# Kernel optimization log

Measured on AMD Instinct MI355X. Metric: run time of the kernel, lower is better.

The kernel has to match this reference:

```python
import jax, jax.numpy as jnp
import numpy as np

B, T, C, H = 8, 2048, 384, 64

def setup_inputs() -> dict:
    key = jax.random.key(0)
    k1, k2, k3, k4 = jax.random.split(key, 4)
    x = jax.random.normal(k1, (B, T, C), dtype=jnp.float32)
    Wq = jax.random.normal(k2, (C, H), dtype=jnp.float32) * (C ** -0.5)
    Wk = jax.random.normal(k3, (C, H), dtype=jnp.float32) * (C ** -0.5)
    Wv = jax.random.normal(k4, (C, H), dtype=jnp.float32) * (C ** -0.5)
    return {"x": x, "Wq": Wq, "Wk": Wk, "Wv": Wv}

def reference(x, Wq, Wk, Wv):
    # x: (B, T, C); projections: (B, T, H)
    Bn, Tn, Cn = x.shape
    q = jnp.einsum('btc,ch->bth', x, Wq)
    k = jnp.einsum('btc,ch->bth', x, Wk)
    v = jnp.einsum('btc,ch->bth', x, Wv)
    # NOTE: source scales by C**-0.5 (embedding dim), not head_size**-0.5
    weights = jnp.einsum('bth,bsh->bts', q, k) * (Cn ** -0.5)  # (B, T, T)
    causal = jnp.tril(jnp.ones((Tn, Tn), dtype=bool))
    weights = jnp.where(causal, weights, -jnp.inf)
    # NOTE: source applies softmax over dim=1 (query/row axis), reproduced faithfully
    weights = jax.nn.softmax(weights, axis=1)
    # dropout omitted (eval-mode reference)
    return jnp.einsum('bts,bsh->bth', weights, v)
```

## Files before the change

kernel.cpp:

```cpp
#include <hip/hip_runtime.h>
#include <hip/hip_bf16.h>
#include <math.h>

#define Bn 8
#define Tn 2048
#define Cn 384
#define Hn 64
#define SCALE2 0.07362241f

using bf16x8 = __attribute__((ext_vector_type(8))) short;
using f32x4  = __attribute__((ext_vector_type(4))) float;
using u32x4  = __attribute__((ext_vector_type(4))) unsigned;

#define MFMA(a, b, c) __builtin_amdgcn_mfma_f32_16x16x32_bf16((a), (b), (c), 0, 0, 0)

static __device__ __forceinline__ short f2bf(float f) {
  unsigned u = __float_as_uint(f);
  u += 0x7fffu + ((u >> 16) & 1u);
  return (short)(u >> 16);
}
static __device__ __forceinline__ float bf2f(short s) {
  return __uint_as_float(((unsigned)(unsigned short)s) << 16);
}
static __device__ __forceinline__ float fexp2(float x) {
#if __has_builtin(__builtin_amdgcn_exp2f)
  return __builtin_amdgcn_exp2f(x);
#else
  return exp2f(x);
#endif
}
static __device__ __forceinline__ float frcp(float x) {
#if __has_builtin(__builtin_amdgcn_rcpf)
  return __builtin_amdgcn_rcpf(x);
#else
  return 1.0f / x;
#endif
}
static __device__ __forceinline__ unsigned pack2(float lo, float hi) {
  return (unsigned)(unsigned short)f2bf(lo) | ((unsigned)(unsigned short)f2bf(hi) << 16);
}
static __device__ __forceinline__ bf16x8 ldp(const unsigned* p) {
  u32x4 t; t[0] = p[0]; t[1] = p[1]; t[2] = p[2]; t[3] = p[3];
  return __builtin_bit_cast(bf16x8, t);
}

__global__ __launch_bounds__(256) void wconv_kernel(
    const float* __restrict__ Wq, const float* __restrict__ Wk,
    const float* __restrict__ Wv, short* __restrict__ WbT,
    float* __restrict__ Lsum) {
  int idx = blockIdx.x * 256 + threadIdx.x;
  if (idx < Bn * Tn) Lsum[idx] = 0.f;
  int n = idx / 384, k = idx - n * 384;
  const float* W = (n < 64) ? Wq : (n < 128) ? Wk : Wv;
  WbT[idx] = f2bf(W[k * 64 + (n & 63)]);
}

__global__ __launch_bounds__(256) void proj_kernel(
    const float* __restrict__ x, const short* __restrict__ WbT,
    short* __restrict__ qb, short* __restrict__ kb, short* __restrict__ vT) {
  __shared__ short xs[16][392];
  __shared__ short vtile[64][20];
  const int tid = threadIdx.x;
  const int t0 = blockIdx.x * 16;
  const float* xb = x + (size_t)t0 * Cn;
  #pragma unroll
  for (int i = 0; i < 6; ++i) {
    int j = tid + i * 256;
    int row = j / 96, colv = (j - row * 96) * 4;
    float4 v = *(const float4*)(xb + row * Cn + colv);
    short4 s4; s4.x = f2bf(v.x); s4.y = f2bf(v.y); s4.z = f2bf(v.z); s4.w = f2bf(v.w);
    *(short4*)(&xs[row][colv]) = s4;
  }
  __syncthreads();
  const int w = tid >> 6, l15 = tid & 15, quad = (tid & 63) >> 4;
  f32x4 acc[3] = {};
  for (int ks = 0; ks < 12; ++ks) {
    bf16x8 a = *(const bf16x8*)(&xs[l15][ks * 32 + quad * 8]);
    #pragma unroll
    for (int cf = 0; cf < 3; ++cf) {
      bf16x8 bfr = *(const bf16x8*)(WbT + (size_t)(48 * w + 16 * cf + l15) * Cn + ks * 32 + quad * 8);
      acc[cf] = MFMA(a, bfr, acc[cf]);
    }
  }
  #pragma unroll
  for (int cf = 0; cf < 3; ++cf) {
    int cbase = 48 * w + 16 * cf, c = cbase + l15;
    #pragma unroll
    for (int r = 0; r < 4; ++r) {
      int row = t0 + quad * 4 + r;
      short val = f2bf(acc[cf][r]);
      if (cbase < 64)       qb[(size_t)row * Hn + c] = val;
      else if (cbase < 128) kb[(size_t)row * Hn + (c - 64)] = val;
      else                  vtile[c - 128][quad * 4 + r] = val;
    }
  }
  __syncthreads();
  const int b = t0 >> 11, t0l = t0 & 2047;
  int h = tid >> 2, tseg = (tid & 3) * 4;
  *(short4*)(vT + ((size_t)(b * Hn + h)) * Tn + t0l + tseg) =
      *(const short4*)(&vtile[h][tseg]);
}

__global__ __launch_bounds__(256) void colstats_kernel(
    const short* __restrict__ qb, const short* __restrict__ kb,
    float* __restrict__ Lsum) {
  const int unit = ((blockIdx.x & 7) << 7) | (blockIdx.x >> 3);
  const int b = unit >> 7, rem = unit & 127;
  const int j = rem >> 3, u = rem & 7;
  const int lo = (u * 33) >> 3, hi = ((u + 1) * 33) >> 3;
  const int big = 32 - j;
  const int tid = threadIdx.x, w = tid >> 6, l15 = tid & 15, quad = (tid & 63) >> 4;
  __shared__ float redl[64][17];

  auto run = [&](const int i, const int k0, const int k1) {
    const int s0 = i << 6;
    float l[4] = {0.f, 0.f, 0.f, 0.f};
    const int n = k1 - k0;
    if (n > 0) {
      bf16x8 bk[8];
      #pragma unroll
      for (int nf = 0; nf < 4; ++nf) {
        const size_t krow = (size_t)(b * Tn + s0 + 16 * nf + l15) * Hn;
        bk[2 * nf]     = *(const bf16x8*)(kb + krow + quad * 8);
        bk[2 * nf + 1] = *(const bf16x8*)(kb + krow + 32 + quad * 8);
      }
      auto cload = [&](bf16x8& A0, bf16x8& A1, int k) {
        size_t ar = (size_t)(b * Tn + ((i + k) << 6) + 16 * w + l15) * Hn;
        A0 = *(const bf16x8*)(qb + ar + quad * 8);
        A1 = *(const bf16x8*)(qb + ar + 32 + quad * 8);
      };
      auto ccomp = [&](bf16x8 A0, bf16x8 A1, int k) {
        f32x4 sc[4] = {};
        #pragma unroll
        for (int nf = 0; nf < 4; ++nf) {
          sc[nf] = MFMA(A0, bk[2 * nf], sc[nf]);
          sc[nf] = MFMA(A1, bk[2 * nf + 1], sc[nf]);
        }
        const bool diag = (k == 0);
        const int tb = ((i + k) << 6) + 16 * w + quad * 4;
        #pragma unroll
        for (int nf = 0; nf < 4; ++nf) {
          int s = s0 + 16 * nf + l15;
          #pragma unroll
          for (int r = 0; r < 4; ++r) {
            float v = sc[nf][r] * SCALE2;
            if (diag && (tb + r) < s) v = -INFINITY;
            l[nf] += fexp2(v);
          }
        }
      };
      bf16x8 a0A, a1A, a0B, a1B, a0C, a1C;
      cload(a0A, a1A, k0);
      if (n > 1) cload(a0B, a1B, k0 + 1);
      if (n > 2) cload(a0C, a1C, k0 + 2);
      int k = k0;
      while (k + 3 < k1) {
        ccomp(a0A, a1A, k);     cload(a0A, a1A, k + 3);
        ccomp(a0B, a1B, k + 1); if (k + 4 < k1) cload(a0B, a1B, k + 4);
        ccomp(a0C, a1C, k + 2); if (k + 5 < k1) cload(a0C, a1C, k + 5);
        k += 3;
      }
      const int rem2 = k1 - k;
      if (rem2 > 0) ccomp(a0A, a1A, k);
      if (rem2 > 1) ccomp(a0B, a1B, k + 1);
      if (rem2 > 2) ccomp(a0C, a1C, k + 2);
    }
    __syncthreads();
    #pragma unroll
    for (int nf = 0; nf < 4; ++nf) redl[16 * nf + l15][w * 4 + quad] = l[nf];
    __syncthreads();
    if (tid < 64) {
      float ls = 0.f;
      #pragma unroll
      for (int q2 = 0; q2 < 16; ++q2) ls += redl[tid][q2];
      atomicAdd(&Lsum[b * Tn + s0 + tid], ls);
    }
  };
  run(j, lo, min(hi, big));
  run(31 - j, max(lo, big) - big, hi - big);
}

__global__ __launch_bounds__(256, 2) void outg_kernel(
    const short* __restrict__ qb, const short* __restrict__ kb,
    const short* __restrict__ vT, const float* __restrict__ Lsum,
    float* __restrict__ out) {
  const int bid = blockIdx.x;
  const int b = bid & 7;
  const int rest = bid >> 3;
  const int tile = 31 - (rest >> 1);
  const int half = rest & 1;
  const int nch = tile + 1;
  const int tid = threadIdx.x, w = tid >> 6, l15 = tid & 15, quad = (tid & 63) >> 4;
  __shared__ unsigned plds[4][512];
  __shared__ float red[4][32][64];
  __shared__ float rcpl[2048];

  const int smax = nch << 6;
  for (int s = tid; s < smax; s += 256)
    rcpl[s] = frcp(Lsum[b * Tn + s]);
  __syncthreads();

  const int swz = (l15 & 7) << 4;
  int wroff[8];
  #pragma unroll
  for (int nf = 0; nf < 4; ++nf)
    #pragma unroll
    for (int p = 0; p < 2; ++p)
      wroff[2 * nf + p] = (l15 * 128 + ((nf * 32 + quad * 8 + p * 4) ^ swz)) >> 2;
  const int rd0 = (l15 * 128 + ((quad * 16) ^ swz)) >> 2;
  const int rd1 = (l15 * 128 + ((64 + quad * 16) ^ swz)) >> 2;
  const size_t QKbase = (size_t)b * Tn * Hn;
  const size_t Vbase  = (size_t)b * Hn * Tn;
  const int tbase = (tile << 6) + (half << 5);
  const int tg0 = tbase + l15;
  const int tg1 = tbase + 16 + l15;

  const size_t qrow0 = QKbase + (size_t)(tbase + l15) * Hn;
  const size_t qrow1 = qrow0 + 16 * Hn;
  const bf16x8 qf00 = *(const bf16x8*)(qb + qrow0 + quad * 8);
  const bf16x8 qf01 = *(const bf16x8*)(qb + qrow0 + 32 + quad * 8);
  const bf16x8 qf10 = *(const bf16x8*)(qb + qrow1 + quad * 8);
  const bf16x8 qf11 = *(const bf16x8*)(qb + qrow1 + 32 + quad * 8);

  f32x4 acc0[4] = {}, acc1[4] = {};
  bf16x8 kfA[8], kfB[8], vf[8];
  auto loadK = [&](bf16x8 (&kf)[8], int ch) {
    const int s0 = ch << 6;
    #pragma unroll
    for (int nf = 0; nf < 4; ++nf) {
      const size_t kr = QKbase + (size_t)(s0 + 16 * nf + l15) * Hn;
      kf[2 * nf]     = *(const bf16x8*)(kb + kr + quad * 8);
      kf[2 * nf + 1] = *(const bf16x8*)(kb + kr + 32 + quad * 8);
    }
  };
  auto loadV = [&](int ch) {
    const int s0 = ch << 6;
    #pragma unroll
    for (int nf = 0; nf < 4; ++nf) {
      const size_t vr = Vbase + (size_t)(16 * nf + l15) * Tn + s0;
      vf[2 * nf]     = *(const bf16x8*)(vT + vr + quad * 8);
      vf[2 * nf + 1] = *(const bf16x8*)(vT + vr + 32 + quad * 8);
    }
  };
  auto strip = [&](const f32x4 (&sc)[4], const float (&rl)[16], int s0,
                   bool diag, int tg, f32x4 (&acc)[4]) {
    #pragma unroll
    for (int nf = 0; nf < 4; ++nf) {
      float ev[4];
      #pragma unroll
      for (int r = 0; r < 4; ++r) {
        float v = sc[nf][r] * SCALE2;
        const int s = s0 + 16 * nf + quad * 4 + r;
        if (diag && tg < s) v = -INFINITY;
        ev[r] = fexp2(v) * rl[nf * 4 + r];
      }
      plds[w][wroff[2 * nf]]     = pack2(ev[0], ev[1]);
      plds[w][wroff[2 * nf + 1]] = pack2(ev[2], ev[3]);
    }
    const bf16x8 a0 = ldp(&plds[w][rd0]);
    const bf16x8 a1 = ldp(&plds[w][rd1]);
    __builtin_amdgcn_s_setprio(1);
    #pragma unroll
    for (int nf = 0; nf < 4; ++nf) {
      acc[nf] = MFMA(a0, vf[2 * nf], acc[nf]);
      acc[nf] = MFMA(a1, vf[2 * nf + 1], acc[nf]);
    }
    __builtin_amdgcn_s_setprio(0);
  };
  auto body = [&](int ch, const bf16x8 (&CUR)[8], bf16x8 (&NXT)[8]) {
    const int s0 = ch << 6;
    const int nx = ch + 4;
    f32x4 sc0[4] = {}, sc1[4] = {};
    __builtin_amdgcn_s_setprio(1);
    #pragma unroll
    for (int nf = 0; nf < 4; ++nf) {
      sc0[nf] = MFMA(CUR[2 * nf], qf00, sc0[nf]);
      sc0[nf] = MFMA(CUR[2 * nf + 1], qf01, sc0[nf]);
    }
    #pragma unroll
    for (int nf = 0; nf < 4; ++nf) {
      sc1[nf] = MFMA(CUR[2 * nf], qf10, sc1[nf]);
      sc1[nf] = MFMA(CUR[2 * nf + 1], qf11, sc1[nf]);
    }
    __builtin_amdgcn_s_setprio(0);
    if (nx < nch) loadK(NXT, nx);
    float rl[16];
    #pragma unroll
    for (int nf = 0; nf < 4; ++nf)
      #pragma unroll
      for (int r = 0; r < 4; ++r)
        rl[nf * 4 + r] = rcpl[s0 + 16 * nf + quad * 4 + r];
    const bool diag = (ch == tile);
    strip(sc0, rl, s0, diag, tg0, acc0);
    strip(sc1, rl, s0, diag, tg1, acc1);
    if (nx < nch) loadV(nx);
  };

  if (w < nch) { loadK(kfA, w); loadV(w); }
  for (int ch = w; ch < nch; ch += 8) {
    body(ch, kfA, kfB);
    if (ch + 4 < nch) body(ch + 4, kfB, kfA);
  }

  #pragma unroll
  for (int nf = 0; nf < 4; ++nf)
    #pragma unroll
    for (int r = 0; r < 4; ++r) {
      red[w][quad * 4 + r][16 * nf + l15]      = acc0[nf][r];
      red[w][16 + quad * 4 + r][16 * nf + l15] = acc1[nf][r];
    }
  __syncthreads();
  {
    const int row = tid >> 3, c8 = (tid & 7) * 8;
    float4 t0 = {0.f, 0.f, 0.f, 0.f}, t1 = {0.f, 0.f, 0.f, 0.f};
    #pragma unroll
    for (int ww = 0; ww < 4; ++ww) {
      float4 s0 = *(const float4*)(&red[ww][row][c8]);
      float4 s1 = *(const float4*)(&red[ww][row][c8 + 4]);
      t0.x += s0.x; t0.y += s0.y; t0.z += s0.z; t0.w += s0.w;
      t1.x += s1.x; t1.y += s1.y; t1.z += s1.z; t1.w += s1.w;
    }
    float* o = &out[QKbase + (size_t)(tbase + row) * Hn + c8];
    *(float4*)(o) = t0;
    *(float4*)(o + 4) = t1;
  }
}

extern "C" void kernel_launch(void* const* d_in, const int* in_sizes, int n_in,
                              void* d_out, int out_size, void* d_ws, size_t ws_size,
                              hipStream_t stream) {
  const float* x  = (const float*)d_in[0];
  const float* Wq = (const float*)d_in[1];
  const float* Wk = (const float*)d_in[2];
  const float* Wv = (const float*)d_in[3];
  char* ws = (char*)d_ws;
  short* qb   = (short*)(ws);
  short* kb   = (short*)(ws + 2097152);
  short* vT   = (short*)(ws + 4194304);
  short* WbT  = (short*)(ws + 6291456);
  float* Lsum = (float*)(ws + 6438912);
  float* outp = (float*)d_out;

  hipLaunchKernelGGL(wconv_kernel, dim3(288), dim3(256), 0, stream, Wq, Wk, Wv, WbT, Lsum);
  hipLaunchKernelGGL(proj_kernel, dim3(Bn * Tn / 16), dim3(256), 0, stream, x, WbT, qb, kb, vT);
  hipLaunchKernelGGL(colstats_kernel, dim3(1024), dim3(256), 0, stream, qb, kb, Lsum);
  hipLaunchKernelGGL(outg_kernel, dim3(512), dim3(256), 0, stream, qb, kb, vT, Lsum, outp);
}
```

Measured before the change: 132.0 us.

## Fold softmax scale into Wq, split colstats finer, shorten prefetch ring

Multiplies Wq by the scale (including log2e) during weight conversion, so the per-score multiply is dropped in both the column-stats and output kernels. The column-stats kernel gets a 2048-block grid with 16 chunks per row-tile, a launch bound of two blocks per unit, a two-deep instead of three-deep q prefetch ring, and raised priority around its MFMA block. It also adds LDS alignment and removes an unused helper. Rounding q to bf16 after scaling slightly changes numerics, and the finer split adds more atomics and duplicate K-fragment loads.

```diff
diff --git a/kernel.cpp b/kernel.cpp
--- a/kernel.cpp
+++ b/kernel.cpp
@@ -18,9 +18,6 @@
   unsigned u = __float_as_uint(f);
   u += 0x7fffu + ((u >> 16) & 1u);
   return (short)(u >> 16);
-}
-static __device__ __forceinline__ float bf2f(short s) {
-  return __uint_as_float(((unsigned)(unsigned short)s) << 16);
 }
 static __device__ __forceinline__ float fexp2(float x) {
 #if __has_builtin(__builtin_amdgcn_exp2f)
@@ -52,7 +49,9 @@
   if (idx < Bn * Tn) Lsum[idx] = 0.f;
   int n = idx / 384, k = idx - n * 384;
   const float* W = (n < 64) ? Wq : (n < 128) ? Wk : Wv;
-  WbT[idx] = f2bf(W[k * 64 + (n & 63)]);
+  float wv = W[k * 64 + (n & 63)];
+  if (n < 64) wv *= SCALE2;
+  WbT[idx] = f2bf(wv);
 }
 
 __global__ __launch_bounds__(256) void proj_kernel(
@@ -101,13 +100,14 @@
       *(const short4*)(&vtile[h][tseg]);
 }
 
-__global__ __launch_bounds__(256) void colstats_kernel(
+__global__ __launch_bounds__(256, 2) void colstats_kernel(
     const short* __restrict__ qb, const short* __restrict__ kb,
     float* __restrict__ Lsum) {
-  const int unit = ((blockIdx.x & 7) << 7) | (blockIdx.x >> 3);
-  const int b = unit >> 7, rem = unit & 127;
-  const int j = rem >> 3, u = rem & 7;
-  const int lo = (u * 33) >> 3, hi = ((u + 1) * 33) >> 3;
+  const int bid = blockIdx.x;
+  const int b = bid & 7;
+  const int rem = bid >> 3;
+  const int j = rem >> 4, u = rem & 15;
+  const int lo = (u * 33) >> 4, hi = ((u + 1) * 33) >> 4;
   const int big = 32 - j;
   const int tid = threadIdx.x, w = tid >> 6, l15 = tid & 15, quad = (tid & 63) >> 4;
   __shared__ float redl[64][17];
@@ -131,11 +131,13 @@
       };
       auto ccomp = [&](bf16x8 A0, bf16x8 A1, int k) {
         f32x4 sc[4] = {};
+        __builtin_amdgcn_s_setprio(1);
         #pragma unroll
         for (int nf = 0; nf < 4; ++nf) {
           sc[nf] = MFMA(A0, bk[2 * nf], sc[nf]);
           sc[nf] = MFMA(A1, bk[2 * nf + 1], sc[nf]);
         }
+        __builtin_amdgcn_s_setprio(0);
         const bool diag = (k == 0);
         const int tb = ((i + k) << 6) + 16 * w + quad * 4;
         #pragma unroll
@@ -143,27 +145,23 @@
           int s = s0 + 16 * nf + l15;
           #pragma unroll
           for (int r = 0; r < 4; ++r) {
-            float v = sc[nf][r] * SCALE2;
+            float v = sc[nf][r];
             if (diag && (tb + r) < s) v = -INFINITY;
             l[nf] += fexp2(v);
           }
         }
       };
-      bf16x8 a0A, a1A, a0B, a1B, a0C, a1C;
+      bf16x8 a0A, a1A, a0B, a1B;
       cload(a0A, a1A, k0);
       if (n > 1) cload(a0B, a1B, k0 + 1);
-      if (n > 2) cload(a0C, a1C, k0 + 2);
       int k = k0;
-      while (k + 3 < k1) {
-        ccomp(a0A, a1A, k);     cload(a0A, a1A, k + 3);
-        ccomp(a0B, a1B, k + 1); if (k + 4 < k1) cload(a0B, a1B, k + 4);
-        ccomp(a0C, a1C, k + 2); if (k + 5 < k1) cload(a0C, a1C, k + 5);
-        k += 3;
+      while (k + 2 < k1) {
+        ccomp(a0A, a1A, k);     cload(a0A, a1A, k + 2);
+        ccomp(a0B, a1B, k + 1); if (k + 3 < k1) cload(a0B, a1B, k + 3);
+        k += 2;
       }
-      const int rem2 = k1 - k;
-      if (rem2 > 0) ccomp(a0A, a1A, k);
-      if (rem2 > 1) ccomp(a0B, a1B, k + 1);
-      if (rem2 > 2) ccomp(a0C, a1C, k + 2);
+      if (k < k1)     ccomp(a0A, a1A, k);
+      if (k + 1 < k1) ccomp(a0B, a1B, k + 1);
     }
     __syncthreads();
     #pragma unroll
@@ -191,9 +189,9 @@
   const int half = rest & 1;
   const int nch = tile + 1;
   const int tid = threadIdx.x, w = tid >> 6, l15 = tid & 15, quad = (tid & 63) >> 4;
-  __shared__ unsigned plds[4][512];
-  __shared__ float red[4][32][64];
-  __shared__ float rcpl[2048];
+  __shared__ alignas(16) unsigned plds[4][512];
+  __shared__ alignas(16) float red[4][32][64];
+  __shared__ alignas(16) float rcpl[2048];
 
   const int smax = nch << 6;
   for (int s = tid; s < smax; s += 256)
@@ -249,7 +247,7 @@
       float ev[4];
       #pragma unroll
       for (int r = 0; r < 4; ++r) {
-        float v = sc[nf][r] * SCALE2;
+        float v = sc[nf][r];
         const int s = s0 + 16 * nf + quad * 4 + r;
         if (diag && tg < s) v = -INFINITY;
         ev[r] = fexp2(v) * rl[nf * 4 + r];
@@ -343,6 +341,6 @@
 
   hipLaunchKernelGGL(wconv_kernel, dim3(288), dim3(256), 0, stream, Wq, Wk, Wv, WbT, Lsum);
   hipLaunchKernelGGL(proj_kernel, dim3(Bn * Tn / 16), dim3(256), 0, stream, x, WbT, qb, kb, vT);
-  hipLaunchKernelGGL(colstats_kernel, dim3(1024), dim3(256), 0, stream, qb, kb, Lsum);
+  hipLaunchKernelGGL(colstats_kernel, dim3(2048), dim3(256), 0, stream, qb, kb, Lsum);
   hipLaunchKernelGGL(outg_kernel, dim3(512), dim3(256), 0, stream, qb, kb, vT, Lsum, outp);
 }
```

After: 135.3 us. 2.5% more time.
